# Kernel optimization log

Hardware: AMD Instinct MI355X
Metric: run time of the kernel (lower is better)

The kernel has to match this reference:

```python
import jax, jax.numpy as jnp
import numpy as np
import math

Q_DIM = 1024
K_DIM = 1024
ATT_DIM = 1024
POS_DIM = 64
B, NQ, NK = 4, 2048, 2048
EPS = 1e-5


def _ln(x, g, b):
    m = jnp.mean(x, axis=-1, keepdims=True)
    v = jnp.var(x, axis=-1, keepdims=True)
    return (x - m) * jax.lax.rsqrt(v + EPS) * g + b


def _sinpos(n, dim):
    # SinPos: exp = 2*arange(dim//2)/dim; pos = p * 10000**-exp; cat(pos, pos+pi/2); sin
    e = 2.0 * jnp.arange(dim // 2, dtype=jnp.float32) / dim      # [dim/2]
    p = jnp.arange(n, dtype=jnp.float32)[:, None]                # [n,1]
    ph = p * jnp.power(10000.0, -e)[None, :]                     # [n,dim/2]
    return jnp.sin(jnp.concatenate([ph, ph + math.pi / 2], axis=1))  # [n,dim]


def setup_inputs() -> dict:
    key = jax.random.key(0)
    ks = jax.random.split(key, 8)
    s = 0.02
    return {
        "q": jax.random.normal(ks[0], (B, NQ, Q_DIM), jnp.float32),
        "k": jax.random.normal(ks[1], (B, NK, K_DIM), jnp.float32),
        "Wq": jax.random.normal(ks[2], (Q_DIM, ATT_DIM), jnp.float32) * s,
        "bq": jnp.zeros((ATT_DIM,), jnp.float32),
        "Wk": jax.random.normal(ks[3], (K_DIM, ATT_DIM), jnp.float32) * s,
        "bk": jnp.zeros((ATT_DIM,), jnp.float32),
        "Wv": jax.random.normal(ks[4], (K_DIM, ATT_DIM), jnp.float32) * s,
        "bv": jnp.zeros((ATT_DIM,), jnp.float32),
        "gq": jnp.ones((ATT_DIM,), jnp.float32), "betaq": jnp.zeros((ATT_DIM,), jnp.float32),
        "gk": jnp.ones((ATT_DIM,), jnp.float32), "betak": jnp.zeros((ATT_DIM,), jnp.float32),
        "gv": jnp.ones((ATT_DIM,), jnp.float32), "betav": jnp.zeros((ATT_DIM,), jnp.float32),
        "Wp": jax.random.normal(ks[5], (POS_DIM, POS_DIM), jnp.float32) * s,
        "bp": jnp.zeros((POS_DIM,), jnp.float32),
    }


def reference(q, k, Wq, bq, Wk, bk, Wv, bv, gq, betaq, gk, betak, gv, betav, Wp, bp):
    qn = _ln(q @ Wq + bq, gq, betaq)          # [B,NQ,D]
    vn = _ln(k @ Wv + bv, gv, betav)          # [B,NK,D]
    kn = _ln(k @ Wk + bk, gk, betak)          # [B,NK,D]
    pos = _sinpos(NK, POS_DIM)                # [NK,P]

    # attention 1: Q=qn, K=kn, V=pos
    s1 = jnp.einsum('bnd,bjd->bnj', qn, kn) * (1.0 / math.sqrt(ATT_DIM))
    a1 = jax.nn.softmax(s1, axis=-1)          # [B,NQ,NK]
    x = jnp.einsum('bnj,jp->bnp', a1, pos)    # [B,NQ,P]

    # pos_net (Linear)
    x = x @ Wp + bp                           # [B,NQ,P]

    # attention 2: Q=x, K=pos, V=vn
    s2 = jnp.einsum('bnp,jp->bnj', x, pos) * (1.0 / math.sqrt(POS_DIM))
    a2 = jax.nn.softmax(s2, axis=-1)          # [B,NQ,NK]
    out = jnp.einsum('bnj,bjd->bnd', a2, vn)  # [B,NQ,D]

    att = jnp.stack([a1, a2], axis=1)         # [B,2,NQ,NK] == torch.cat over head dim
    return out, att
```

## Files before the change

kernel.cpp:

```cpp
#include <hip/hip_runtime.h>
#include <math.h>
#include <stdint.h>


typedef _Float16 f16;
typedef _Float16 f16x4 __attribute__((ext_vector_type(4)));
typedef _Float16 f16x8 __attribute__((ext_vector_type(8)));
typedef float f32x4 __attribute__((ext_vector_type(4)));

static constexpr int CB  = 4;
static constexpr int CNQ = 2048;
static constexpr int CNK = 2048;
static constexpr int CD  = 1024;
static constexpr int CP  = 64;

static __device__ __forceinline__ void async16(const f16* gp, f16* lp) {
  __builtin_amdgcn_global_load_lds(
      (const __attribute__((address_space(1))) void*)(uintptr_t)gp,
      (__attribute__((address_space(3))) void*)(uint32_t)(uintptr_t)lp,
      16, 0, 0);
}

__global__ __launch_bounds__(256) void pos_kernel(f16* __restrict__ posb,
                                                  f16* __restrict__ posTb) {
  int tid = blockIdx.x * 256 + threadIdx.x;
  int p = tid >> 11;
  int j = tid & (CNK - 1);
  int i = p & 31;
  float ph = (float)j * powf(10000.0f, -(float)i * (1.0f / 32.0f));
  float v = (p < 32) ? sinf(ph) : cosf(ph);
  posb[j * CP + p]   = (f16)v;
  posTb[p * CNK + j] = (f16)v;
}

__global__ __launch_bounds__(256) void cvt2_kernel(const float* __restrict__ a,
                                                   const float* __restrict__ b,
                                                   f16* __restrict__ oa,
                                                   f16* __restrict__ ob) {
  const int NF4 = CB * CNQ * CD / 4;
  int tid = blockIdx.x * 256 + threadIdx.x;
  const float* src = (tid < NF4) ? a : b;
  f16* dst = (tid < NF4) ? oa : ob;
  int i = (tid < NF4) ? tid : tid - NF4;
  float4 v = reinterpret_cast<const float4*>(src)[i];
  f16x4 o = {(f16)v.x, (f16)v.y, (f16)v.z, (f16)v.w};
  reinterpret_cast<f16x4*>(dst)[i] = o;
}

__global__ __launch_bounds__(256) void cvtWT_kernel(
    const float* __restrict__ Wq, const float* __restrict__ Wk,
    const float* __restrict__ Wv, f16* __restrict__ WqT, f16* __restrict__ WkvT) {
  __shared__ float t[64][65];
  const float* W = (blockIdx.z == 0) ? Wq : (blockIdx.z == 1) ? Wk : Wv;
  f16* WT = (blockIdx.z == 0) ? WqT : (blockIdx.z == 1) ? WkvT : WkvT + 1024 * 1024;
  int k0 = blockIdx.x * 64, n0 = blockIdx.y * 64;
  int tx = threadIdx.x & 63, ty = threadIdx.x >> 6;
#pragma unroll
  for (int i = 0; i < 16; i++)
    t[ty + 4 * i][tx] = W[(size_t)(k0 + ty + 4 * i) * CD + n0 + tx];
  __syncthreads();
#pragma unroll
  for (int i = 0; i < 16; i++)
    WT[(size_t)(n0 + 4 * i + ty) * CD + k0 + tx] = (f16)t[tx][ty + 4 * i];
}

__global__ __launch_bounds__(256) void transpose_kernel(const f16* __restrict__ in,
                                                        f16* __restrict__ out,
                                                        int ldi) {
  __shared__ f16 t[64][65];
  int n0 = blockIdx.x * 64, d0 = blockIdx.y * 64;
  size_t ibase = (size_t)blockIdx.z * CNK * ldi;
  size_t obase = (size_t)blockIdx.z * CNK * CD;
  int tx = threadIdx.x & 63, ty = threadIdx.x >> 6;
#pragma unroll
  for (int i = 0; i < 16; i++)
    t[ty + 4 * i][tx] = in[ibase + (size_t)(n0 + ty + 4 * i) * ldi + d0 + tx];
  __syncthreads();
#pragma unroll
  for (int i = 0; i < 16; i++)
    out[obase + (size_t)(d0 + ty + 4 * i) * CNK + n0 + tx] = t[tx][ty + 4 * i];
}

template <int BM, int BN, int EPI>
__global__ __launch_bounds__(512) void gemm8(
    const f16* __restrict__ A, const f16* __restrict__ Bt, void* __restrict__ C,
    int K, int lda, int ldb, int ldc, size_t sA, size_t sB, size_t sC,
    float scale, int gx, int gy, void* __restrict__ aux) {
  constexpr int FM = BM / 32;
  constexpr int FN = BN / 64;
  constexpr int MH = (FN == 4) ? 2 : 1;
  constexpr int FMC = FM / MH;
  constexpr int TI = (BM + BN) / 64;
  __shared__ __attribute__((aligned(16))) f16 sm[2][(BM + BN) * 64];
  __shared__ float psum[BM];

  const int nwg = gridDim.x;
  const int qch = nwg >> 3;
  const int swz = (blockIdx.x & 7) * qch + (blockIdx.x >> 3);
  const int bz = swz / (gx * gy);
  const int rem = swz - bz * gx * gy;
  const int by = rem / gx;
  const int bx = rem - by * gx;
  const int m0 = bx * BM, n0 = by * BN;

  const f16* Ab = A + sA * bz;
  const f16* Bb = Bt + sB * bz;
  const int tid = threadIdx.x;
  const int lane = tid & 63, wid = tid >> 6;
  const int wr = wid >> 2, wc = wid & 3;
  const int lrow = lane & 15, kg = lane >> 4;

  auto stage = [&](int i, int kt, int buf) {
    const int s = i * 512 + tid;
    const int row = s >> 3;
    const int cb = (s & 7) << 4;
    const int scb = cb ^ ((row & 7) << 4);
    const f16* src = (i < BM / 64)
        ? Ab + (size_t)(m0 + row) * lda + kt * 64 + (scb >> 1)
        : Bb + (size_t)(n0 + row - BM) * ldb + kt * 64 + (scb >> 1);
    async16(src, &sm[buf][(size_t)s * 8]);
  };

  f32x4 acc[FM][FN] = {};
  const int NT = K >> 6;

#pragma unroll
  for (int i = 0; i < TI; i++) stage(i, 0, 0);

  for (int t = 0; t < NT; ++t) {
    const int cur = t & 1;
    if (t + 1 < NT) {
#pragma unroll
      for (int i = 0; i < TI; i++) stage(i, t + 1, cur ^ 1);
      if constexpr (TI == 8) asm volatile("s_waitcnt vmcnt(8)" ::: "memory");
      else                   asm volatile("s_waitcnt vmcnt(6)" ::: "memory");
    } else {
      asm volatile("s_waitcnt vmcnt(0)" ::: "memory");
    }
    __builtin_amdgcn_s_barrier();

    const f16* smA = sm[cur];
    const f16* smB = sm[cur] + BM * 64;
    f16x8 bf[2][FN];
#pragma unroll
    for (int p = 0; p < 2 * MH; ++p) {
      const int kk = p / MH, mh = p % MH;
      const int Cb = kk * 64 + kg * 16;
      f16x8 af[FMC];
#pragma unroll
      for (int m = 0; m < FMC; ++m) {
        const int ar = wr * (BM / 2) + mh * (FMC * 16) + m * 16 + lrow;
        af[m] = *reinterpret_cast<const f16x8*>(
            &smA[ar * 64 + ((Cb ^ ((ar & 7) << 4)) >> 1)]);
      }
      if (mh == 0) {
#pragma unroll
        for (int n = 0; n < FN; ++n) {
          const int br = wc * (BN / 4) + n * 16 + lrow;
          bf[kk][n] = *reinterpret_cast<const f16x8*>(
              &smB[br * 64 + ((Cb ^ ((br & 7) << 4)) >> 1)]);
        }
      }
      __builtin_amdgcn_s_barrier();
      __builtin_amdgcn_s_setprio(1);
#pragma unroll
      for (int m = 0; m < FMC; ++m)
#pragma unroll
        for (int n = 0; n < FN; ++n)
          acc[mh * FMC + m][n] = __builtin_amdgcn_mfma_f32_16x16x32_f16(
              af[m], bf[kk][n], acc[mh * FMC + m][n], 0, 0, 0);
      __builtin_amdgcn_s_setprio(0);
      __builtin_amdgcn_s_barrier();
    }
  }

  const int rbase = wr * (BM / 2) + (lane >> 4) * 4;
  const int cbase = wc * (BN / 4) + lrow;

  if constexpr (EPI == 1 || EPI == 2) {
    f16* st = (f16*)sm;
    if constexpr (EPI == 2) { if (tid < BM) psum[tid] = 0.f; }
#pragma unroll
    for (int mg = 0; mg < FM; mg++)
#pragma unroll
      for (int n = 0; n < FN; n++)
#pragma unroll
        for (int r = 0; r < 4; r++) {
          float v = acc[mg][n][r];
          if constexpr (EPI == 2) v = __expf(v * scale);
          st[(rbase + mg * 16 + r) * BN + cbase + n * 16] = (f16)v;
        }
    __syncthreads();
    constexpr int CH = BM * BN / (512 * 8);
    f16* Cp = (f16*)C + sC * bz;
#pragma unroll
    for (int c = 0; c < CH; c++) {
      const int idx = c * 512 + tid;
      const int row = idx / (BN / 8);
      const int cole = (idx % (BN / 8)) * 8;
      f16x8 v = *reinterpret_cast<const f16x8*>(&st[row * BN + cole]);
      *reinterpret_cast<f16x8*>(Cp + (size_t)(m0 + row) * ldc + n0 + cole) = v;
      if constexpr (EPI == 2) {
        float p = 0.f;
#pragma unroll
        for (int j = 0; j < 8; j++) p += (float)v[j];
#pragma unroll
        for (int o = 1; o < 32; o <<= 1) p += __shfl_xor(p, o);
        if ((lane & 31) == 0) atomicAdd(&psum[row], p);
      }
    }
    if constexpr (EPI == 2) {
      __syncthreads();
      if (tid < BM) {
        float* PS = (float*)aux;
        const int rowg = bz * (gx * BM) + m0 + tid;
        PS[(size_t)by * (CB * CNQ) + rowg] = psum[tid];
      }
    }
  } else {
    const float* inv = (const float*)aux;
    float* st = (float*)sm;
    float* Cp = (float*)C + sC * bz;
#pragma unroll
    for (int half = 0; half < 2; half++) {
      __syncthreads();
      if (wr == half) {
#pragma unroll
        for (int mg = 0; mg < FM; mg++)
#pragma unroll
          for (int r = 0; r < 4; r++) {
            const int rloc = (lane >> 4) * 4 + mg * 16 + r;
            const float iv = inv[bz * (gx * BM) + m0 + half * (BM / 2) + rloc];
#pragma unroll
            for (int n = 0; n < FN; n++)
              st[rloc * BN + cbase + n * 16] = acc[mg][n][r] * scale * iv;
          }
      }
      __syncthreads();
      constexpr int CH = (BM / 2) * BN / (512 * 4);
#pragma unroll
      for (int c = 0; c < CH; c++) {
        const int idx = c * 512 + tid;
        const int row = idx / (BN / 4);
        const int cole = (idx % (BN / 4)) * 4;
        float4 v = *reinterpret_cast<const float4*>(&st[row * BN + cole]);
        *reinterpret_cast<float4*>(
            Cp + (size_t)(m0 + half * (BM / 2) + row) * ldc + n0 + cole) = v;
      }
    }
  }
}

template <int BM, int BN>
__global__ __launch_bounds__(256) void gemm_nt(
    const f16* __restrict__ A, const f16* __restrict__ Bt, float* __restrict__ C,
    int K, int lda, int ldb, int ldc) {
  constexpr int FM = BM / 32;
  constexpr int FN = BN / 32;
  constexpr int NA = BM / 16, NTOT = NA + BN / 16;
  __shared__ __attribute__((aligned(16))) f16 As[BM * 32];
  __shared__ __attribute__((aligned(16))) f16 Bs[BN * 32];

  const int lane = threadIdx.x & 63;
  const int wave = threadIdx.x >> 6;
  const int wr = wave >> 1, wc = wave & 1;
  const int m0 = blockIdx.x * BM, n0 = blockIdx.y * BN;
  const int srow = lane >> 2;
  const int scol = (lane & 3) * 8;
  const int lrow = lane & 15;
  const int kg = lane >> 4;

  f32x4 acc[FM][FN] = {};

  for (int k0 = 0; k0 < K; k0 += 32) {
    __syncthreads();
#pragma unroll
    for (int i = wave; i < NTOT; i += 4) {
      if (i < NA)
        async16(A + (size_t)(m0 + i * 16 + srow) * lda + k0 + scol, &As[i * 512]);
      else
        async16(Bt + (size_t)(n0 + (i - NA) * 16 + srow) * ldb + k0 + scol,
                &Bs[(i - NA) * 512]);
    }
    __syncthreads();

    f16x8 af[FM], bfr[FN];
#pragma unroll
    for (int m = 0; m < FM; m++)
      af[m] = *reinterpret_cast<const f16x8*>(
          &As[(wr * (BM / 2) + m * 16 + lrow) * 32 + kg * 8]);
#pragma unroll
    for (int n = 0; n < FN; n++)
      bfr[n] = *reinterpret_cast<const f16x8*>(
          &Bs[(wc * (BN / 2) + n * 16 + lrow) * 32 + kg * 8]);
#pragma unroll
    for (int m = 0; m < FM; m++)
#pragma unroll
      for (int n = 0; n < FN; n++)
        acc[m][n] = __builtin_amdgcn_mfma_f32_16x16x32_f16(af[m], bfr[n], acc[m][n], 0, 0, 0);
  }

  const int crow = m0 + wr * (BM / 2) + (lane >> 4) * 4;
  const int ccol = n0 + wc * (BN / 2) + (lane & 15);
#pragma unroll
  for (int m = 0; m < FM; m++)
#pragma unroll
    for (int n = 0; n < FN; n++)
#pragma unroll
      for (int r = 0; r < 4; r++)
        C[(size_t)(crow + m * 16 + r) * ldc + ccol + n * 16] = acc[m][n][r];
}

__global__ __launch_bounds__(256) void ln_kernel(
    f16* __restrict__ buf, const float* __restrict__ bias,
    const float* __restrict__ g, const float* __restrict__ beta) {
  __shared__ float rs_[4], rq_[4];
  const int t = threadIdx.x;
  f16* rp = buf + (size_t)blockIdx.x * CD;
  f16x4 v = *reinterpret_cast<const f16x4*>(rp + t * 4);
  float y[4], s = 0.f, q = 0.f;
#pragma unroll
  for (int j = 0; j < 4; j++) {
    y[j] = (float)v[j] + bias[t * 4 + j];
    s += y[j]; q += y[j] * y[j];
  }
#pragma unroll
  for (int o = 32; o; o >>= 1) { s += __shfl_xor(s, o); q += __shfl_xor(q, o); }
  if ((t & 63) == 0) { rs_[t >> 6] = s; rq_[t >> 6] = q; }
  __syncthreads();
  s = rs_[0] + rs_[1] + rs_[2] + rs_[3];
  q = rq_[0] + rq_[1] + rq_[2] + rq_[3];
  const float mean = s * (1.0f / CD);
  const float rstd = rsqrtf(q * (1.0f / CD) - mean * mean + 1e-5f);
  f16x4 o;
#pragma unroll
  for (int j = 0; j < 4; j++) {
    int c = t * 4 + j;
    o[j] = (f16)((y[j] - mean) * rstd * g[c] + beta[c]);
  }
  *reinterpret_cast<f16x4*>(rp + t * 4) = o;
}

__global__ __launch_bounds__(256) void lnkv_kernel(
    f16* __restrict__ buf,
    const float* __restrict__ bk, const float* __restrict__ gk, const float* __restrict__ bek,
    const float* __restrict__ bv, const float* __restrict__ gv, const float* __restrict__ bev) {
  __shared__ float rs_[4], rq_[4];
  const int z = blockIdx.y;
  const float* bias = z ? bv : bk;
  const float* g    = z ? gv : gk;
  const float* beta = z ? bev : bek;
  const int t = threadIdx.x;
  f16* rp = buf + (size_t)blockIdx.x * 2048 + z * 1024;
  f16x4 v = *reinterpret_cast<const f16x4*>(rp + t * 4);
  float y[4], s = 0.f, q = 0.f;
#pragma unroll
  for (int j = 0; j < 4; j++) {
    y[j] = (float)v[j] + bias[t * 4 + j];
    s += y[j]; q += y[j] * y[j];
  }
#pragma unroll
  for (int o = 32; o; o >>= 1) { s += __shfl_xor(s, o); q += __shfl_xor(q, o); }
  if ((t & 63) == 0) { rs_[t >> 6] = s; rq_[t >> 6] = q; }
  __syncthreads();
  s = rs_[0] + rs_[1] + rs_[2] + rs_[3];
  q = rq_[0] + rq_[1] + rq_[2] + rq_[3];
  const float mean = s * (1.0f / CD);
  const float rstd = rsqrtf(q * (1.0f / CD) - mean * mean + 1e-5f);
  f16x4 o;
#pragma unroll
  for (int j = 0; j < 4; j++) {
    int c = t * 4 + j;
    o[j] = (f16)((y[j] - mean) * rstd * g[c] + beta[c]);
  }
  *reinterpret_cast<f16x4*>(rp + t * 4) = o;
}

__global__ __launch_bounds__(256) void norm_kernel(
    const f16* __restrict__ e, const float* __restrict__ ps,
    const float* __restrict__ invin, float* __restrict__ invout,
    float* __restrict__ att, int head) {
  const int row = blockIdx.x;
  const int b = row >> 11, n = row & (CNQ - 1);
  float iv;
  if (ps) {
    float s = 0.f;
#pragma unroll
    for (int j = 0; j < 8; j++) s += ps[j * (CB * CNQ) + row];
    iv = 1.0f / s;
    if (threadIdx.x == 0) invout[row] = iv;
  } else {
    iv = invin[row];
  }
  const int t = threadIdx.x;
  float* rp = att + ((size_t)((b << 1) + head) * CNQ + n) * CNK;
  f16x8 v = *reinterpret_cast<const f16x8*>(e + (size_t)row * CNK + t * 8);
  float4 w0 = {(float)v[0] * iv, (float)v[1] * iv, (float)v[2] * iv, (float)v[3] * iv};
  float4 w1 = {(float)v[4] * iv, (float)v[5] * iv, (float)v[6] * iv, (float)v[7] * iv};
  reinterpret_cast<float4*>(rp)[t * 2]     = w0;
  reinterpret_cast<float4*>(rp)[t * 2 + 1] = w1;
}

__global__ __launch_bounds__(128) void attn2_kernel(
    const float* __restrict__ x, const float* __restrict__ Wp,
    const float* __restrict__ bp, const f16* __restrict__ posb,
    const float* __restrict__ inv1, f16* __restrict__ e2,
    float* __restrict__ inv2) {
  __shared__ float xs[32 * 64];
  __shared__ float Wps[64 * 64];
  __shared__ __attribute__((aligned(16))) f16 xpb[32 * 64];
  __shared__ __attribute__((aligned(16))) f16 elds[2][16 * 64];
  const int tid = threadIdx.x, l = tid & 63, w = tid >> 6;
  const int r0 = blockIdx.x * 32;
#pragma unroll
  for (int i = 0; i < 16; i++) {
    const int row = w * 16 + i;
    xs[row * 64 + l] = x[(size_t)(r0 + row) * CP + l] * inv1[r0 + row];
  }
#pragma unroll
  for (int i = w; i < 64; i += 2) Wps[i * 64 + l] = Wp[i * 64 + l];
  const float bpl = bp[l];
  __syncthreads();
  const int rb = w * 16;
#pragma unroll 2
  for (int i = 0; i < 16; i++) {
    float a = bpl;
#pragma unroll 8
    for (int p = 0; p < 64; p++) a = fmaf(xs[(rb + i) * 64 + p], Wps[p * 64 + l], a);
    xpb[(rb + i) * 64 + l] = (f16)a;
  }
  asm volatile("s_waitcnt lgkmcnt(0)" ::: "memory");
  const f16x8 af0 = *reinterpret_cast<const f16x8*>(&xpb[(rb + (l & 15)) * 64 + (l >> 4) * 8]);
  const f16x8 af1 = *reinterpret_cast<const f16x8*>(&xpb[(rb + (l & 15)) * 64 + 32 + (l >> 4) * 8]);
  float rs[4] = {0.f, 0.f, 0.f, 0.f};
  f16* eb = e2 + (size_t)(r0 + rb) * CNK;
  for (int jt = 0; jt < CNK / 64; jt++) {
#pragma unroll
    for (int q4 = 0; q4 < 4; q4++) {
      const int j = jt * 64 + q4 * 16 + (l & 15);
      const f16* pp = posb + (size_t)j * CP + (l >> 4) * 8;
      f16x8 b0 = *reinterpret_cast<const f16x8*>(pp);
      f16x8 b1 = *reinterpret_cast<const f16x8*>(pp + 32);
      f32x4 c = {};
      c = __builtin_amdgcn_mfma_f32_16x16x32_f16(af0, b0, c, 0, 0, 0);
      c = __builtin_amdgcn_mfma_f32_16x16x32_f16(af1, b1, c, 0, 0, 0);
#pragma unroll
      for (int r = 0; r < 4; r++) {
        float ev = __expf(c[r] * 0.125f);
        rs[r] += ev;
        elds[w][((l >> 4) * 4 + r) * 64 + q4 * 16 + (l & 15)] = (f16)ev;
      }
    }
    asm volatile("s_waitcnt lgkmcnt(0)" ::: "memory");
    f16x8 h0 = *reinterpret_cast<const f16x8*>(&elds[w][(l >> 2) * 64 + (l & 3) * 16]);
    f16x8 h1 = *reinterpret_cast<const f16x8*>(&elds[w][(l >> 2) * 64 + (l & 3) * 16 + 8]);
    f16* op = eb + (size_t)(l >> 2) * CNK + jt * 64 + (l & 3) * 16;
    *reinterpret_cast<f16x8*>(op)     = h0;
    *reinterpret_cast<f16x8*>(op + 8) = h1;
    asm volatile("s_waitcnt lgkmcnt(0)" ::: "memory");
  }
#pragma unroll
  for (int r = 0; r < 4; r++) {
#pragma unroll
    for (int o = 1; o < 16; o <<= 1) rs[r] += __shfl_xor(rs[r], o);
    if ((l & 15) == 0) inv2[r0 + rb + (l >> 4) * 4 + r] = 1.0f / rs[r];
  }
}

extern "C" void kernel_launch(void* const* d_in, const int* in_sizes, int n_in,
                              void* d_out, int out_size, void* d_ws, size_t ws_size,
                              hipStream_t stream) {
  (void)in_sizes; (void)n_in; (void)out_size; (void)ws_size;
  const float* q    = (const float*)d_in[0];
  const float* k    = (const float*)d_in[1];
  const float* Wq   = (const float*)d_in[2];
  const float* bq   = (const float*)d_in[3];
  const float* Wk   = (const float*)d_in[4];
  const float* bk   = (const float*)d_in[5];
  const float* Wv   = (const float*)d_in[6];
  const float* bv   = (const float*)d_in[7];
  const float* gq   = (const float*)d_in[8];
  const float* betaq= (const float*)d_in[9];
  const float* gk   = (const float*)d_in[10];
  const float* betak= (const float*)d_in[11];
  const float* gv   = (const float*)d_in[12];
  const float* betav= (const float*)d_in[13];
  const float* Wp   = (const float*)d_in[14];
  const float* bp   = (const float*)d_in[15];

  float* out = (float*)d_out;
  float* att = out + (size_t)CB * CNQ * CD;
  char* ws = (char*)d_ws;
  const size_t MB = 1ull << 20;

  f16* q16   = (f16*)(ws);
  f16* k16   = (f16*)(ws + 16 * MB);
  f16* e1    = (f16*)(ws);
  f16* e2    = (f16*)(ws);
  f16* WqT   = (f16*)(ws + 32 * MB);
  f16* WkvT  = (f16*)(ws + 34 * MB);
  f16* posb  = (f16*)(ws + 38 * MB);
  f16* posTb = (f16*)(ws + 38 * MB + 256 * 1024);
  float* xw  = (float*)(ws + 38 * MB + 512 * 1024);
  float* PS  = (float*)(ws + 40 * MB + 512 * 1024);
  float* inv1= (float*)(ws + 40 * MB + 768 * 1024);
  float* inv2= (float*)(ws + 40 * MB + 800 * 1024);
  f16* tmpq  = (f16*)(ws + 41 * MB);
  f16* tmp2  = (f16*)(ws + 57 * MB);
  f16* vnT   = (f16*)(ws + 89 * MB);
  f16* qn = tmpq;
  f16* kn = tmp2;
  f16* vn = tmp2 + 1024;

  pos_kernel<<<(CP * CNK) / 256, 256, 0, stream>>>(posb, posTb);
  cvt2_kernel<<<2 * (CB * CNQ * CD / 4) / 256, 256, 0, stream>>>(q, k, q16, k16);
  cvtWT_kernel<<<dim3(16, 16, 3), 256, 0, stream>>>(Wq, Wk, Wv, WqT, WkvT);

  gemm8<256, 128, 1><<<256, 512, 0, stream>>>(q16, WqT, tmpq, CD, CD, CD, CD,
                                              0, 0, 0, 1.f, 32, 8, nullptr);
  ln_kernel<<<CB * CNQ, 256, 0, stream>>>(tmpq, bq, gq, betaq);
  gemm8<256, 256, 1><<<256, 512, 0, stream>>>(k16, WkvT, tmp2, CD, CD, CD, 2048,
                                              0, 0, 0, 1.f, 32, 8, nullptr);
  lnkv_kernel<<<dim3(CB * CNK, 2), 256, 0, stream>>>(tmp2, bk, gk, betak, bv, gv, betav);
  transpose_kernel<<<dim3(CNK / 64, CD / 64, CB), 256, 0, stream>>>(vn, vnT, 2048);

  gemm8<256, 256, 2><<<256, 512, 0, stream>>>(qn, kn, e1, CD, CD, 2048, CNK,
      (size_t)CNQ * CD, (size_t)CNK * 2048, (size_t)CNQ * CNK, 0.03125f, 8, 8, PS);
  norm_kernel<<<CB * CNQ, 256, 0, stream>>>(e1, PS, nullptr, inv1, att, 0);

  gemm_nt<64, 64><<<dim3(CB * CNQ / 64, 1, 1), 256, 0, stream>>>(
      e1, posTb, xw, CNK, CNK, CNK, CP);
  attn2_kernel<<<CB * CNQ / 32, 128, 0, stream>>>(xw, Wp, bp, posb, inv1, e2, inv2);
  norm_kernel<<<CB * CNQ, 256, 0, stream>>>(e2, nullptr, inv2, nullptr, att, 1);

  gemm8<256, 128, 3><<<256, 512, 0, stream>>>(e2, vnT, out, CNK, CNK, CNK, CD,
      (size_t)CNQ * CNK, (size_t)CD * CNK, (size_t)CNQ * CD, 1.f, 8, 8, inv2);
}
```

Before: 335.1 us.

## Merge input GEMMs, fuse LN launches, split-K x GEMM, fuse attn2 normalization

The q and k/v projection GEMMs become one 768-block launch, and the three layernorms run in a single kernel. The x = a1@pos GEMM is split into two K halves to expose more blocks, and attn2 now stages a full 32x2048 row block in LDS. That lets it normalize in place, writing both the fp32 att head and the normalized fp16 e2, which removes the separate norm pass. The output GEMM then no longer rescales by inv2. This trades launches and extra passes over the large attention matrices for very large LDS use in attn2 (about 132 KB per block), which lowers occupancy.

Measured after the change: 324.1 us. 1.03x faster.

```diff
diff --git a/kernel.cpp b/kernel.cpp
--- a/kernel.cpp
+++ b/kernel.cpp
@@ -81,30 +81,14 @@
     out[obase + (size_t)(d0 + ty + 4 * i) * CNK + n0 + tx] = t[tx][ty + 4 * i];
 }
 
-template <int BM, int BN, int EPI>
-__global__ __launch_bounds__(512) void gemm8(
-    const f16* __restrict__ A, const f16* __restrict__ Bt, void* __restrict__ C,
-    int K, int lda, int ldb, int ldc, size_t sA, size_t sB, size_t sC,
-    float scale, int gx, int gy, void* __restrict__ aux) {
-  constexpr int FM = BM / 32;
-  constexpr int FN = BN / 64;
-  constexpr int MH = (FN == 4) ? 2 : 1;
-  constexpr int FMC = FM / MH;
+template <int BM, int BN>
+__device__ __forceinline__ void gemm_core(
+    const f16* __restrict__ Ab, const f16* __restrict__ Bb,
+    int lda, int ldb, int K, int m0, int n0, f16* sm,
+    f32x4 (&acc)[BM / 32][BN / 64]) {
+  constexpr int FM = BM / 32, FN = BN / 64;
   constexpr int TI = (BM + BN) / 64;
-  __shared__ __attribute__((aligned(16))) f16 sm[2][(BM + BN) * 64];
-  __shared__ float psum[BM];
-
-  const int nwg = gridDim.x;
-  const int qch = nwg >> 3;
-  const int swz = (blockIdx.x & 7) * qch + (blockIdx.x >> 3);
-  const int bz = swz / (gx * gy);
-  const int rem = swz - bz * gx * gy;
-  const int by = rem / gx;
-  const int bx = rem - by * gx;
-  const int m0 = bx * BM, n0 = by * BN;
-
-  const f16* Ab = A + sA * bz;
-  const f16* Bb = Bt + sB * bz;
+  constexpr int bufsz = (BM + BN) * 64;
   const int tid = threadIdx.x;
   const int lane = tid & 63, wid = tid >> 6;
   const int wr = wid >> 2, wc = wid & 3;
@@ -118,12 +102,10 @@
     const f16* src = (i < BM / 64)
         ? Ab + (size_t)(m0 + row) * lda + kt * 64 + (scb >> 1)
         : Bb + (size_t)(n0 + row - BM) * ldb + kt * 64 + (scb >> 1);
-    async16(src, &sm[buf][(size_t)s * 8]);
+    async16(src, &sm[buf * bufsz + s * 8]);
   };
 
-  f32x4 acc[FM][FN] = {};
   const int NT = K >> 6;
-
 #pragma unroll
   for (int i = 0; i < TI; i++) stage(i, 0, 0);
 
@@ -139,184 +121,209 @@
     }
     __builtin_amdgcn_s_barrier();
 
-    const f16* smA = sm[cur];
-    const f16* smB = sm[cur] + BM * 64;
-    f16x8 bf[2][FN];
-#pragma unroll
-    for (int p = 0; p < 2 * MH; ++p) {
-      const int kk = p / MH, mh = p % MH;
+    const f16* smA = sm + cur * bufsz;
+    const f16* smB = smA + BM * 64;
+#pragma unroll
+    for (int kk = 0; kk < 2; ++kk) {
       const int Cb = kk * 64 + kg * 16;
-      f16x8 af[FMC];
-#pragma unroll
-      for (int m = 0; m < FMC; ++m) {
-        const int ar = wr * (BM / 2) + mh * (FMC * 16) + m * 16 + lrow;
+      f16x8 af[FM], bf[FN];
+#pragma unroll
+      for (int m = 0; m < FM; ++m) {
+        const int ar = wr * (BM / 2) + m * 16 + lrow;
         af[m] = *reinterpret_cast<const f16x8*>(
             &smA[ar * 64 + ((Cb ^ ((ar & 7) << 4)) >> 1)]);
       }
-      if (mh == 0) {
-#pragma unroll
-        for (int n = 0; n < FN; ++n) {
-          const int br = wc * (BN / 4) + n * 16 + lrow;
-          bf[kk][n] = *reinterpret_cast<const f16x8*>(
-              &smB[br * 64 + ((Cb ^ ((br & 7) << 4)) >> 1)]);
-        }
+#pragma unroll
+      for (int n = 0; n < FN; ++n) {
+        const int br = wc * (BN / 4) + n * 16 + lrow;
+        bf[n] = *reinterpret_cast<const f16x8*>(
+            &smB[br * 64 + ((Cb ^ ((br & 7) << 4)) >> 1)]);
       }
       __builtin_amdgcn_s_barrier();
       __builtin_amdgcn_s_setprio(1);
 #pragma unroll
-      for (int m = 0; m < FMC; ++m)
+      for (int m = 0; m < FM; ++m)
 #pragma unroll
         for (int n = 0; n < FN; ++n)
-          acc[mh * FMC + m][n] = __builtin_amdgcn_mfma_f32_16x16x32_f16(
-              af[m], bf[kk][n], acc[mh * FMC + m][n], 0, 0, 0);
+          acc[m][n] = __builtin_amdgcn_mfma_f32_16x16x32_f16(af[m], bf[n], acc[m][n], 0, 0, 0);
       __builtin_amdgcn_s_setprio(0);
       __builtin_amdgcn_s_barrier();
     }
   }
-
+}
+
+template <int BM, int BN>
+__device__ __forceinline__ void epi_f16(
+    f32x4 (&acc)[BM / 32][BN / 64], f16* sm, f16* Cp, int ldc, int m0, int n0) {
+  const int tid = threadIdx.x, lane = tid & 63, wid = tid >> 6;
+  const int wr = wid >> 2, wc = wid & 3;
   const int rbase = wr * (BM / 2) + (lane >> 4) * 4;
-  const int cbase = wc * (BN / 4) + lrow;
-
-  if constexpr (EPI == 1 || EPI == 2) {
-    f16* st = (f16*)sm;
-    if constexpr (EPI == 2) { if (tid < BM) psum[tid] = 0.f; }
-#pragma unroll
-    for (int mg = 0; mg < FM; mg++)
-#pragma unroll
-      for (int n = 0; n < FN; n++)
+  const int cbase = wc * (BN / 4) + (lane & 15);
+  __syncthreads();
+#pragma unroll
+  for (int mg = 0; mg < BM / 32; mg++)
+#pragma unroll
+    for (int n = 0; n < BN / 64; n++)
+#pragma unroll
+      for (int r = 0; r < 4; r++)
+        sm[(rbase + mg * 16 + r) * BN + cbase + n * 16] = (f16)acc[mg][n][r];
+  __syncthreads();
+  constexpr int CH = BM * BN / (512 * 8);
+#pragma unroll
+  for (int c = 0; c < CH; c++) {
+    const int idx = c * 512 + tid;
+    const int row = idx / (BN / 8);
+    const int cole = (idx % (BN / 8)) * 8;
+    f16x8 v = *reinterpret_cast<const f16x8*>(&sm[row * BN + cole]);
+    *reinterpret_cast<f16x8*>(Cp + (size_t)(m0 + row) * ldc + n0 + cole) = v;
+  }
+}
+
+template <int BM, int BN>
+__device__ __forceinline__ void epi_exp(
+    f32x4 (&acc)[BM / 32][BN / 64], f16* sm, float* psum, f16* Cp, int ldc,
+    int m0, int n0, float scale, float* PSrow) {
+  const int tid = threadIdx.x, lane = tid & 63, wid = tid >> 6;
+  const int wr = wid >> 2, wc = wid & 3;
+  const int rbase = wr * (BM / 2) + (lane >> 4) * 4;
+  const int cbase = wc * (BN / 4) + (lane & 15);
+  __syncthreads();
+  if (tid < BM) psum[tid] = 0.f;
+#pragma unroll
+  for (int mg = 0; mg < BM / 32; mg++)
+#pragma unroll
+    for (int n = 0; n < BN / 64; n++)
+#pragma unroll
+      for (int r = 0; r < 4; r++)
+        sm[(rbase + mg * 16 + r) * BN + cbase + n * 16] =
+            (f16)__expf(acc[mg][n][r] * scale);
+  __syncthreads();
+  constexpr int CH = BM * BN / (512 * 8);
+#pragma unroll
+  for (int c = 0; c < CH; c++) {
+    const int idx = c * 512 + tid;
+    const int row = idx / (BN / 8);
+    const int cole = (idx % (BN / 8)) * 8;
+    f16x8 v = *reinterpret_cast<const f16x8*>(&sm[row * BN + cole]);
+    *reinterpret_cast<f16x8*>(Cp + (size_t)(m0 + row) * ldc + n0 + cole) = v;
+    float p = 0.f;
+#pragma unroll
+    for (int j = 0; j < 8; j++) p += (float)v[j];
+#pragma unroll
+    for (int o = 1; o < 32; o <<= 1) p += __shfl_xor(p, o);
+    if ((lane & 31) == 0) atomicAdd(&psum[row], p);
+  }
+  __syncthreads();
+  if (tid < BM) PSrow[tid] = psum[tid];
+}
+
+template <int BM, int BN>
+__device__ __forceinline__ void epi_f32(
+    f32x4 (&acc)[BM / 32][BN / 64], f16* smh, float* Cp, int ldc, int m0, int n0) {
+  float* st = (float*)smh;
+  const int tid = threadIdx.x, lane = tid & 63, wid = tid >> 6;
+  const int wr = wid >> 2, wc = wid & 3;
+  const int cbase = wc * (BN / 4) + (lane & 15);
+#pragma unroll
+  for (int half = 0; half < 2; half++) {
+    __syncthreads();
+    if (wr == half) {
+#pragma unroll
+      for (int mg = 0; mg < BM / 32; mg++)
 #pragma unroll
         for (int r = 0; r < 4; r++) {
-          float v = acc[mg][n][r];
-          if constexpr (EPI == 2) v = __expf(v * scale);
-          st[(rbase + mg * 16 + r) * BN + cbase + n * 16] = (f16)v;
+          const int rloc = (lane >> 4) * 4 + mg * 16 + r;
+#pragma unroll
+          for (int n = 0; n < BN / 64; n++)
+            st[rloc * BN + cbase + n * 16] = acc[mg][n][r];
         }
+    }
     __syncthreads();
-    constexpr int CH = BM * BN / (512 * 8);
-    f16* Cp = (f16*)C + sC * bz;
+    constexpr int CH = (BM / 2) * BN / (512 * 4);
 #pragma unroll
     for (int c = 0; c < CH; c++) {
       const int idx = c * 512 + tid;
-      const int row = idx / (BN / 8);
-      const int cole = (idx % (BN / 8)) * 8;
-      f16x8 v = *reinterpret_cast<const f16x8*>(&st[row * BN + cole]);
-      *reinterpret_cast<f16x8*>(Cp + (size_t)(m0 + row) * ldc + n0 + cole) = v;
-      if constexpr (EPI == 2) {
-        float p = 0.f;
-#pragma unroll
-        for (int j = 0; j < 8; j++) p += (float)v[j];
-#pragma unroll
-        for (int o = 1; o < 32; o <<= 1) p += __shfl_xor(p, o);
-        if ((lane & 31) == 0) atomicAdd(&psum[row], p);
-      }
+      const int row = idx / (BN / 4);
+      const int cole = (idx % (BN / 4)) * 4;
+      float4 v = *reinterpret_cast<const float4*>(&st[row * BN + cole]);
+      *reinterpret_cast<float4*>(
+          Cp + (size_t)(m0 + half * (BM / 2) + row) * ldc + n0 + cole) = v;
     }
-    if constexpr (EPI == 2) {
-      __syncthreads();
-      if (tid < BM) {
-        float* PS = (float*)aux;
-        const int rowg = bz * (gx * BM) + m0 + tid;
-        PS[(size_t)by * (CB * CNQ) + rowg] = psum[tid];
-      }
-    }
+  }
+}
+
+__global__ __launch_bounds__(512) void gemmIn_kernel(
+    const f16* __restrict__ q16, const f16* __restrict__ WqT, f16* __restrict__ tmpq,
+    const f16* __restrict__ k16, const f16* __restrict__ WkvT, f16* __restrict__ tmp2) {
+  __shared__ __attribute__((aligned(16))) f16 sm[2][(256 + 128) * 64];
+  const int b = blockIdx.x;
+  const int swz = (b & 7) * 96 + (b >> 3);
+  const f16 *A, *B;
+  f16* C;
+  int ldc, m0, n0;
+  if (swz < 256) {
+    const int by = swz >> 5, bx = swz & 31;
+    A = q16; B = WqT; C = tmpq; ldc = 1024; m0 = bx * 256; n0 = by * 128;
   } else {
-    const float* inv = (const float*)aux;
-    float* st = (float*)sm;
-    float* Cp = (float*)C + sC * bz;
-#pragma unroll
-    for (int half = 0; half < 2; half++) {
-      __syncthreads();
-      if (wr == half) {
-#pragma unroll
-        for (int mg = 0; mg < FM; mg++)
-#pragma unroll
-          for (int r = 0; r < 4; r++) {
-            const int rloc = (lane >> 4) * 4 + mg * 16 + r;
-            const float iv = inv[bz * (gx * BM) + m0 + half * (BM / 2) + rloc];
-#pragma unroll
-            for (int n = 0; n < FN; n++)
-              st[rloc * BN + cbase + n * 16] = acc[mg][n][r] * scale * iv;
-          }
-      }
-      __syncthreads();
-      constexpr int CH = (BM / 2) * BN / (512 * 4);
-#pragma unroll
-      for (int c = 0; c < CH; c++) {
-        const int idx = c * 512 + tid;
-        const int row = idx / (BN / 4);
-        const int cole = (idx % (BN / 4)) * 4;
-        float4 v = *reinterpret_cast<const float4*>(&st[row * BN + cole]);
-        *reinterpret_cast<float4*>(
-            Cp + (size_t)(m0 + half * (BM / 2) + row) * ldc + n0 + cole) = v;
-      }
-    }
-  }
-}
-
-template <int BM, int BN>
-__global__ __launch_bounds__(256) void gemm_nt(
-    const f16* __restrict__ A, const f16* __restrict__ Bt, float* __restrict__ C,
-    int K, int lda, int ldb, int ldc) {
-  constexpr int FM = BM / 32;
-  constexpr int FN = BN / 32;
-  constexpr int NA = BM / 16, NTOT = NA + BN / 16;
-  __shared__ __attribute__((aligned(16))) f16 As[BM * 32];
-  __shared__ __attribute__((aligned(16))) f16 Bs[BN * 32];
-
-  const int lane = threadIdx.x & 63;
-  const int wave = threadIdx.x >> 6;
-  const int wr = wave >> 1, wc = wave & 1;
-  const int m0 = blockIdx.x * BM, n0 = blockIdx.y * BN;
-  const int srow = lane >> 2;
-  const int scol = (lane & 3) * 8;
-  const int lrow = lane & 15;
-  const int kg = lane >> 4;
-
-  f32x4 acc[FM][FN] = {};
-
-  for (int k0 = 0; k0 < K; k0 += 32) {
-    __syncthreads();
-#pragma unroll
-    for (int i = wave; i < NTOT; i += 4) {
-      if (i < NA)
-        async16(A + (size_t)(m0 + i * 16 + srow) * lda + k0 + scol, &As[i * 512]);
-      else
-        async16(Bt + (size_t)(n0 + (i - NA) * 16 + srow) * ldb + k0 + scol,
-                &Bs[(i - NA) * 512]);
-    }
-    __syncthreads();
-
-    f16x8 af[FM], bfr[FN];
-#pragma unroll
-    for (int m = 0; m < FM; m++)
-      af[m] = *reinterpret_cast<const f16x8*>(
-          &As[(wr * (BM / 2) + m * 16 + lrow) * 32 + kg * 8]);
-#pragma unroll
-    for (int n = 0; n < FN; n++)
-      bfr[n] = *reinterpret_cast<const f16x8*>(
-          &Bs[(wc * (BN / 2) + n * 16 + lrow) * 32 + kg * 8]);
-#pragma unroll
-    for (int m = 0; m < FM; m++)
-#pragma unroll
-      for (int n = 0; n < FN; n++)
-        acc[m][n] = __builtin_amdgcn_mfma_f32_16x16x32_f16(af[m], bfr[n], acc[m][n], 0, 0, 0);
-  }
-
-  const int crow = m0 + wr * (BM / 2) + (lane >> 4) * 4;
-  const int ccol = n0 + wc * (BN / 2) + (lane & 15);
-#pragma unroll
-  for (int m = 0; m < FM; m++)
-#pragma unroll
-    for (int n = 0; n < FN; n++)
-#pragma unroll
-      for (int r = 0; r < 4; r++)
-        C[(size_t)(crow + m * 16 + r) * ldc + ccol + n * 16] = acc[m][n][r];
-}
-
-__global__ __launch_bounds__(256) void ln_kernel(
-    f16* __restrict__ buf, const float* __restrict__ bias,
-    const float* __restrict__ g, const float* __restrict__ beta) {
+    const int idx = swz - 256;
+    const int by = idx >> 5, bx = idx & 31;
+    A = k16; B = WkvT; C = tmp2; ldc = 2048; m0 = bx * 256; n0 = by * 128;
+  }
+  f32x4 acc[8][2] = {};
+  gemm_core<256, 128>(A, B, 1024, 1024, 1024, m0, n0, &sm[0][0], acc);
+  epi_f16<256, 128>(acc, &sm[0][0], C, ldc, m0, n0);
+}
+
+__global__ __launch_bounds__(512) void gemmS1_kernel(
+    const f16* __restrict__ qn, const f16* __restrict__ kn,
+    f16* __restrict__ e1, float* __restrict__ PS) {
+  __shared__ __attribute__((aligned(16))) f16 sm[2][(256 + 256) * 64];
+  __shared__ float psum[256];
+  const int b = blockIdx.x;
+  const int swz = (b & 7) * 32 + (b >> 3);
+  const int bz = swz >> 6;
+  const int rem = swz & 63;
+  const int by = rem >> 3, bx = rem & 7;
+  const int m0 = bx * 256, n0 = by * 256;
+  const f16* Ab = qn + (size_t)bz * 2048 * 1024;
+  const f16* Bb = kn + (size_t)bz * 2048 * 2048;
+  f16* Cp = e1 + (size_t)bz * 2048 * 2048;
+  f32x4 acc[8][4] = {};
+  gemm_core<256, 256>(Ab, Bb, 1024, 2048, 1024, m0, n0, &sm[0][0], acc);
+  epi_exp<256, 256>(acc, &sm[0][0], psum, Cp, 2048, m0, n0, 0.03125f,
+                    PS + (size_t)by * 8192 + bz * 2048 + m0);
+}
+
+__global__ __launch_bounds__(512) void gemmOut_kernel(
+    const f16* __restrict__ e2, const f16* __restrict__ vnT, float* __restrict__ out) {
+  __shared__ __attribute__((aligned(16))) f16 sm[2][(256 + 128) * 64];
+  const int b = blockIdx.x;
+  const int swz = (b & 7) * 32 + (b >> 3);
+  const int bz = swz >> 6;
+  const int rem = swz & 63;
+  const int by = rem >> 3, bx = rem & 7;
+  const int m0 = bx * 256, n0 = by * 128;
+  const f16* Ab = e2 + (size_t)bz * 2048 * 2048;
+  const f16* Bb = vnT + (size_t)bz * 1024 * 2048;
+  float* Cp = out + (size_t)bz * 2048 * 1024;
+  f32x4 acc[8][2] = {};
+  gemm_core<256, 128>(Ab, Bb, 2048, 2048, 2048, m0, n0, &sm[0][0], acc);
+  epi_f32<256, 128>(acc, &sm[0][0], Cp, 1024, m0, n0);
+}
+
+__global__ __launch_bounds__(256) void ln3_kernel(
+    f16* __restrict__ tmpq, f16* __restrict__ tmp2,
+    const float* __restrict__ bq, const float* __restrict__ gq, const float* __restrict__ beq,
+    const float* __restrict__ bk, const float* __restrict__ gk, const float* __restrict__ bek,
+    const float* __restrict__ bv, const float* __restrict__ gv, const float* __restrict__ bev) {
   __shared__ float rs_[4], rq_[4];
+  const int z = blockIdx.y;
+  f16* rp;
+  const float *bias, *g, *beta;
+  if (z == 0)      { rp = tmpq + (size_t)blockIdx.x * 1024;        bias = bq; g = gq; beta = beq; }
+  else if (z == 1) { rp = tmp2 + (size_t)blockIdx.x * 2048;        bias = bk; g = gk; beta = bek; }
+  else             { rp = tmp2 + (size_t)blockIdx.x * 2048 + 1024; bias = bv; g = gv; beta = bev; }
   const int t = threadIdx.x;
-  f16* rp = buf + (size_t)blockIdx.x * CD;
   f16x4 v = *reinterpret_cast<const f16x4*>(rp + t * 4);
   float y[4], s = 0.f, q = 0.f;
 #pragma unroll
@@ -341,81 +348,94 @@
   *reinterpret_cast<f16x4*>(rp + t * 4) = o;
 }
 
-__global__ __launch_bounds__(256) void lnkv_kernel(
-    f16* __restrict__ buf,
-    const float* __restrict__ bk, const float* __restrict__ gk, const float* __restrict__ bek,
-    const float* __restrict__ bv, const float* __restrict__ gv, const float* __restrict__ bev) {
-  __shared__ float rs_[4], rq_[4];
-  const int z = blockIdx.y;
-  const float* bias = z ? bv : bk;
-  const float* g    = z ? gv : gk;
-  const float* beta = z ? bev : bek;
-  const int t = threadIdx.x;
-  f16* rp = buf + (size_t)blockIdx.x * 2048 + z * 1024;
-  f16x4 v = *reinterpret_cast<const f16x4*>(rp + t * 4);
-  float y[4], s = 0.f, q = 0.f;
-#pragma unroll
-  for (int j = 0; j < 4; j++) {
-    y[j] = (float)v[j] + bias[t * 4 + j];
-    s += y[j]; q += y[j] * y[j];
-  }
-#pragma unroll
-  for (int o = 32; o; o >>= 1) { s += __shfl_xor(s, o); q += __shfl_xor(q, o); }
-  if ((t & 63) == 0) { rs_[t >> 6] = s; rq_[t >> 6] = q; }
-  __syncthreads();
-  s = rs_[0] + rs_[1] + rs_[2] + rs_[3];
-  q = rq_[0] + rq_[1] + rq_[2] + rq_[3];
-  const float mean = s * (1.0f / CD);
-  const float rstd = rsqrtf(q * (1.0f / CD) - mean * mean + 1e-5f);
-  f16x4 o;
-#pragma unroll
-  for (int j = 0; j < 4; j++) {
-    int c = t * 4 + j;
-    o[j] = (f16)((y[j] - mean) * rstd * g[c] + beta[c]);
-  }
-  *reinterpret_cast<f16x4*>(rp + t * 4) = o;
-}
-
-__global__ __launch_bounds__(256) void norm_kernel(
-    const f16* __restrict__ e, const float* __restrict__ ps,
-    const float* __restrict__ invin, float* __restrict__ invout,
-    float* __restrict__ att, int head) {
+__global__ __launch_bounds__(256) void norm1_kernel(
+    const f16* __restrict__ e1, const float* __restrict__ PS,
+    float* __restrict__ inv1, float* __restrict__ att) {
   const int row = blockIdx.x;
   const int b = row >> 11, n = row & (CNQ - 1);
-  float iv;
-  if (ps) {
-    float s = 0.f;
-#pragma unroll
-    for (int j = 0; j < 8; j++) s += ps[j * (CB * CNQ) + row];
-    iv = 1.0f / s;
-    if (threadIdx.x == 0) invout[row] = iv;
-  } else {
-    iv = invin[row];
-  }
+  float s = 0.f;
+#pragma unroll
+  for (int j = 0; j < 8; j++) s += PS[j * (CB * CNQ) + row];
+  const float iv = 1.0f / s;
+  if (threadIdx.x == 0) inv1[row] = iv;
   const int t = threadIdx.x;
-  float* rp = att + ((size_t)((b << 1) + head) * CNQ + n) * CNK;
-  f16x8 v = *reinterpret_cast<const f16x8*>(e + (size_t)row * CNK + t * 8);
+  float* rp = att + ((size_t)(b << 1) * CNQ + n) * CNK;
+  f16x8 v = *reinterpret_cast<const f16x8*>(e1 + (size_t)row * CNK + t * 8);
   float4 w0 = {(float)v[0] * iv, (float)v[1] * iv, (float)v[2] * iv, (float)v[3] * iv};
   float4 w1 = {(float)v[4] * iv, (float)v[5] * iv, (float)v[6] * iv, (float)v[7] * iv};
   reinterpret_cast<float4*>(rp)[t * 2]     = w0;
   reinterpret_cast<float4*>(rp)[t * 2 + 1] = w1;
 }
 
+__global__ __launch_bounds__(256) void xgemm_kernel(
+    const f16* __restrict__ e1, const f16* __restrict__ posTb, float* __restrict__ xw) {
+  constexpr int BM = 64, BN = 64;
+  __shared__ __attribute__((aligned(16))) f16 As[BM * 32];
+  __shared__ __attribute__((aligned(16))) f16 Bs[BN * 32];
+  const int lane = threadIdx.x & 63;
+  const int wave = threadIdx.x >> 6;
+  const int wr = wave >> 1, wc = wave & 1;
+  const int m0 = blockIdx.x * BM;
+  const int kbase = blockIdx.z * 1024;
+  const int srow = lane >> 2;
+  const int scol = (lane & 3) * 8;
+  const int lrow = lane & 15;
+  const int kg = lane >> 4;
+  f32x4 acc[2][2] = {};
+  for (int k0 = 0; k0 < 1024; k0 += 32) {
+    __syncthreads();
+#pragma unroll
+    for (int i = wave; i < 8; i += 4) {
+      if (i < 4)
+        async16(e1 + (size_t)(m0 + i * 16 + srow) * CNK + kbase + k0 + scol, &As[i * 512]);
+      else
+        async16(posTb + (size_t)((i - 4) * 16 + srow) * CNK + kbase + k0 + scol,
+                &Bs[(i - 4) * 512]);
+    }
+    __syncthreads();
+    f16x8 af[2], bfr[2];
+#pragma unroll
+    for (int m = 0; m < 2; m++)
+      af[m] = *reinterpret_cast<const f16x8*>(&As[(wr * 32 + m * 16 + lrow) * 32 + kg * 8]);
+#pragma unroll
+    for (int n = 0; n < 2; n++)
+      bfr[n] = *reinterpret_cast<const f16x8*>(&Bs[(wc * 32 + n * 16 + lrow) * 32 + kg * 8]);
+#pragma unroll
+    for (int m = 0; m < 2; m++)
+#pragma unroll
+      for (int n = 0; n < 2; n++)
+        acc[m][n] = __builtin_amdgcn_mfma_f32_16x16x32_f16(af[m], bfr[n], acc[m][n], 0, 0, 0);
+  }
+  float* Cp = xw + (size_t)blockIdx.z * (CB * CNQ) * CP;
+  const int crow = m0 + wr * 32 + (lane >> 4) * 4;
+  const int ccol = wc * 32 + (lane & 15);
+#pragma unroll
+  for (int m = 0; m < 2; m++)
+#pragma unroll
+    for (int n = 0; n < 2; n++)
+#pragma unroll
+      for (int r = 0; r < 4; r++)
+        Cp[(size_t)(crow + m * 16 + r) * CP + ccol + n * 16] = acc[m][n][r];
+}
+
 __global__ __launch_bounds__(128) void attn2_kernel(
-    const float* __restrict__ x, const float* __restrict__ Wp,
+    const float* __restrict__ xw, const float* __restrict__ Wp,
     const float* __restrict__ bp, const f16* __restrict__ posb,
     const float* __restrict__ inv1, f16* __restrict__ e2,
-    float* __restrict__ inv2) {
-  __shared__ float xs[32 * 64];
-  __shared__ float Wps[64 * 64];
-  __shared__ __attribute__((aligned(16))) f16 xpb[32 * 64];
-  __shared__ __attribute__((aligned(16))) f16 elds[2][16 * 64];
+    float* __restrict__ att) {
+  __shared__ __attribute__((aligned(16))) f16 shm[32 * 2048 + 32 * 64];
+  __shared__ float rsum[32];
+  f16* e2lds = shm;
+  f16* xpb = shm + 32 * 2048;
+  float* xs = (float*)shm;
+  float* Wps = (float*)shm + 32 * 64;
   const int tid = threadIdx.x, l = tid & 63, w = tid >> 6;
   const int r0 = blockIdx.x * 32;
 #pragma unroll
   for (int i = 0; i < 16; i++) {
     const int row = w * 16 + i;
-    xs[row * 64 + l] = x[(size_t)(r0 + row) * CP + l] * inv1[r0 + row];
+    const size_t gi = (size_t)(r0 + row) * CP + l;
+    xs[row * 64 + l] = (xw[gi] + xw[(size_t)(CB * CNQ) * CP + gi]) * inv1[r0 + row];
   }
 #pragma unroll
   for (int i = w; i < 64; i += 2) Wps[i * 64 + l] = Wp[i * 64 + l];
@@ -429,11 +449,10 @@
     for (int p = 0; p < 64; p++) a = fmaf(xs[(rb + i) * 64 + p], Wps[p * 64 + l], a);
     xpb[(rb + i) * 64 + l] = (f16)a;
   }
-  asm volatile("s_waitcnt lgkmcnt(0)" ::: "memory");
+  __syncthreads();
   const f16x8 af0 = *reinterpret_cast<const f16x8*>(&xpb[(rb + (l & 15)) * 64 + (l >> 4) * 8]);
   const f16x8 af1 = *reinterpret_cast<const f16x8*>(&xpb[(rb + (l & 15)) * 64 + 32 + (l >> 4) * 8]);
   float rs[4] = {0.f, 0.f, 0.f, 0.f};
-  f16* eb = e2 + (size_t)(r0 + rb) * CNK;
   for (int jt = 0; jt < CNK / 64; jt++) {
 #pragma unroll
     for (int q4 = 0; q4 < 4; q4++) {
@@ -448,22 +467,40 @@
       for (int r = 0; r < 4; r++) {
         float ev = __expf(c[r] * 0.125f);
         rs[r] += ev;
-        elds[w][((l >> 4) * 4 + r) * 64 + q4 * 16 + (l & 15)] = (f16)ev;
+        e2lds[(rb + (l >> 4) * 4 + r) * 2048 + j] = (f16)ev;
       }
     }
-    asm volatile("s_waitcnt lgkmcnt(0)" ::: "memory");
-    f16x8 h0 = *reinterpret_cast<const f16x8*>(&elds[w][(l >> 2) * 64 + (l & 3) * 16]);
-    f16x8 h1 = *reinterpret_cast<const f16x8*>(&elds[w][(l >> 2) * 64 + (l & 3) * 16 + 8]);
-    f16* op = eb + (size_t)(l >> 2) * CNK + jt * 64 + (l & 3) * 16;
-    *reinterpret_cast<f16x8*>(op)     = h0;
-    *reinterpret_cast<f16x8*>(op + 8) = h1;
-    asm volatile("s_waitcnt lgkmcnt(0)" ::: "memory");
   }
 #pragma unroll
   for (int r = 0; r < 4; r++) {
 #pragma unroll
     for (int o = 1; o < 16; o <<= 1) rs[r] += __shfl_xor(rs[r], o);
-    if ((l & 15) == 0) inv2[r0 + rb + (l >> 4) * 4 + r] = 1.0f / rs[r];
+    if ((l & 15) == 0) rsum[rb + (l >> 4) * 4 + r] = rs[r];
+  }
+  __syncthreads();
+  const int b = r0 >> 11, nloc = r0 & (CNQ - 1);
+  float* attb = att + ((size_t)((b << 1) + 1) * CNQ + nloc) * CNK;
+  f16* e2b = e2 + (size_t)r0 * CNK;
+  for (int row = 0; row < 32; row++) {
+    const float iv = 1.0f / rsum[row];
+    const f16x8 a0 = *reinterpret_cast<const f16x8*>(&e2lds[row * 2048 + tid * 16]);
+    const f16x8 a1 = *reinterpret_cast<const f16x8*>(&e2lds[row * 2048 + tid * 16 + 8]);
+    float4 w0 = {(float)a0[0] * iv, (float)a0[1] * iv, (float)a0[2] * iv, (float)a0[3] * iv};
+    float4 w1 = {(float)a0[4] * iv, (float)a0[5] * iv, (float)a0[6] * iv, (float)a0[7] * iv};
+    float4 w2 = {(float)a1[0] * iv, (float)a1[1] * iv, (float)a1[2] * iv, (float)a1[3] * iv};
+    float4 w3 = {(float)a1[4] * iv, (float)a1[5] * iv, (float)a1[6] * iv, (float)a1[7] * iv};
+    float* ap = attb + (size_t)row * CNK + tid * 16;
+    reinterpret_cast<float4*>(ap)[0] = w0;
+    reinterpret_cast<float4*>(ap)[1] = w1;
+    reinterpret_cast<float4*>(ap)[2] = w2;
+    reinterpret_cast<float4*>(ap)[3] = w3;
+    f16x8 h0 = {(f16)w0.x, (f16)w0.y, (f16)w0.z, (f16)w0.w,
+                (f16)w1.x, (f16)w1.y, (f16)w1.z, (f16)w1.w};
+    f16x8 h1 = {(f16)w2.x, (f16)w2.y, (f16)w2.z, (f16)w2.w,
+                (f16)w3.x, (f16)w3.y, (f16)w3.z, (f16)w3.w};
+    f16* ep = e2b + (size_t)row * CNK + tid * 16;
+    *reinterpret_cast<f16x8*>(ep)     = h0;
+    *reinterpret_cast<f16x8*>(ep + 8) = h1;
   }
 }
 
@@ -502,12 +539,11 @@
   f16* posb  = (f16*)(ws + 38 * MB);
   f16* posTb = (f16*)(ws + 38 * MB + 256 * 1024);
   float* xw  = (float*)(ws + 38 * MB + 512 * 1024);
-  float* PS  = (float*)(ws + 40 * MB + 512 * 1024);
-  float* inv1= (float*)(ws + 40 * MB + 768 * 1024);
-  float* inv2= (float*)(ws + 40 * MB + 800 * 1024);
-  f16* tmpq  = (f16*)(ws + 41 * MB);
-  f16* tmp2  = (f16*)(ws + 57 * MB);
-  f16* vnT   = (f16*)(ws + 89 * MB);
+  float* PS  = (float*)(ws + 42 * MB + 512 * 1024);
+  float* inv1= (float*)(ws + 42 * MB + 768 * 1024);
+  f16* tmpq  = (f16*)(ws + 43 * MB);
+  f16* tmp2  = (f16*)(ws + 59 * MB);
+  f16* vnT   = (f16*)(ws + 91 * MB);
   f16* qn = tmpq;
   f16* kn = tmp2;
   f16* vn = tmp2 + 1024;
@@ -516,23 +552,16 @@
   cvt2_kernel<<<2 * (CB * CNQ * CD / 4) / 256, 256, 0, stream>>>(q, k, q16, k16);
   cvtWT_kernel<<<dim3(16, 16, 3), 256, 0, stream>>>(Wq, Wk, Wv, WqT, WkvT);
 
-  gemm8<256, 128, 1><<<256, 512, 0, stream>>>(q16, WqT, tmpq, CD, CD, CD, CD,
-                                              0, 0, 0, 1.f, 32, 8, nullptr);
-  ln_kernel<<<CB * CNQ, 256, 0, stream>>>(tmpq, bq, gq, betaq);
-  gemm8<256, 256, 1><<<256, 512, 0, stream>>>(k16, WkvT, tmp2, CD, CD, CD, 2048,
-                                              0, 0, 0, 1.f, 32, 8, nullptr);
-  lnkv_kernel<<<dim3(CB * CNK, 2), 256, 0, stream>>>(tmp2, bk, gk, betak, bv, gv, betav);
+  gemmIn_kernel<<<768, 512, 0, stream>>>(q16, WqT, tmpq, k16, WkvT, tmp2);
+  ln3_kernel<<<dim3(CB * CNQ, 3), 256, 0, stream>>>(
+      tmpq, tmp2, bq, gq, betaq, bk, gk, betak, bv, gv, betav);
   transpose_kernel<<<dim3(CNK / 64, CD / 64, CB), 256, 0, stream>>>(vn, vnT, 2048);
 
-  gemm8<256, 256, 2><<<256, 512, 0, stream>>>(qn, kn, e1, CD, CD, 2048, CNK,
-      (size_t)CNQ * CD, (size_t)CNK * 2048, (size_t)CNQ * CNK, 0.03125f, 8, 8, PS);
-  norm_kernel<<<CB * CNQ, 256, 0, stream>>>(e1, PS, nullptr, inv1, att, 0);
-
-  gemm_nt<64, 64><<<dim3(CB * CNQ / 64, 1, 1), 256, 0, stream>>>(
-      e1, posTb, xw, CNK, CNK, CNK, CP);
-  attn2_kernel<<<CB * CNQ / 32, 128, 0, stream>>>(xw, Wp, bp, posb, inv1, e2, inv2);
-  norm_kernel<<<CB * CNQ, 256, 0, stream>>>(e2, nullptr, inv2, nullptr, att, 1);
-
-  gemm8<256, 128, 3><<<256, 512, 0, stream>>>(e2, vnT, out, CNK, CNK, CNK, CD,
-      (size_t)CNQ * CNK, (size_t)CD * CNK, (size_t)CNQ * CD, 1.f, 8, 8, inv2);
-}
+  gemmS1_kernel<<<256, 512, 0, stream>>>(qn, kn, e1, PS);
+  norm1_kernel<<<CB * CNQ, 256, 0, stream>>>(e1, PS, inv1, att);
+
+  xgemm_kernel<<<dim3(CB * CNQ / 64, 1, 2), 256, 0, stream>>>(e1, posTb, xw);
+  attn2_kernel<<<CB * CNQ / 32, 128, 0, stream>>>(xw, Wp, bp, posb, inv1, e2, att);
+
+  gemmOut_kernel<<<256, 512, 0, stream>>>(e2, vnT, out);
+}
```
